# Kernel optimization log

Measured on AMD Instinct MI355X. Metric: run time of the kernel, lower is better.

The kernel has to match this reference:

```python
import jax, jax.numpy as jnp
import numpy as np

N = 50000   # node_count
D = 64      # dim_in (also GCN hidden, GRU hidden, top-k k)
E = 800000  # num_edges


def setup_inputs() -> dict:
    key = jax.random.key(0)
    ks = jax.random.split(key, 10)
    s = 1.0 / np.sqrt(D)
    return {
        "x": jax.random.normal(ks[0], (N, D), jnp.float32),
        "edge_index": jax.random.randint(ks[1], (2, E), 0, N, dtype=jnp.int64),
        "edge_weight": jax.random.uniform(ks[2], (E,), jnp.float32),
        # TopKPooling projection vector p
        "pool_p": jax.random.normal(ks[3], (D,), jnp.float32) * s,
        # EvolveGCNH initial weight (GRU hidden state h0), [D, D]
        "init_W": jax.random.normal(ks[4], (D, D), jnp.float32) * s,
        # GRU params, torch gate order (r, z, n)
        "gru_Wih": jax.random.normal(ks[5], (3 * D, D), jnp.float32) * s,
        "gru_Whh": jax.random.normal(ks[6], (3 * D, D), jnp.float32) * s,
        "gru_bih": jax.random.normal(ks[7], (3 * D,), jnp.float32) * s,
        "gru_bhh": jax.random.normal(ks[8], (3 * D,), jnp.float32) * s,
        # final Linear(D, 1)
        "lin_W": jax.random.normal(ks[9], (1, D), jnp.float32) * s,
        "lin_b": jnp.zeros((1,), jnp.float32),
    }


def reference(x, edge_index, edge_weight, pool_p, init_W,
              gru_Wih, gru_Whh, gru_bih, gru_bhh, lin_W, lin_b):
    n, d = x.shape
    # ---- TopKPooling: k = ceil((D/N) * N) = D nodes ----
    score = (x @ pool_p) / jnp.linalg.norm(pool_p)          # [N]
    vals, perm = jax.lax.top_k(score, d)                    # descending, k = D
    x_tilde = x[perm] * jnp.tanh(vals)[:, None]             # [D, D]
    # ---- one GRU step: batch = D pooled nodes, hidden = D, h0 = init_W ----
    gi = x_tilde @ gru_Wih.T + gru_bih                      # [D, 3D]
    gh = init_W @ gru_Whh.T + gru_bhh                       # [D, 3D]
    i_r, i_z, i_n = jnp.split(gi, 3, axis=-1)
    h_r, h_z, h_n = jnp.split(gh, 3, axis=-1)
    r = jax.nn.sigmoid(i_r + h_r)
    z = jax.nn.sigmoid(i_z + h_z)
    nn_ = jnp.tanh(i_n + r * h_n)
    W = (1.0 - z) * nn_ + z * init_W                        # evolved GCN weight [D, D]
    # ---- GCNConv_Fixed_W: add self-loops + symmetric norm + scatter ----
    loop = jnp.arange(n)
    row = jnp.concatenate([edge_index[0], loop])            # sources
    col = jnp.concatenate([edge_index[1], loop])            # targets
    w = jnp.concatenate([edge_weight, jnp.ones((n,), x.dtype)])
    deg = jax.ops.segment_sum(w, col, num_segments=n)
    deg_safe = jnp.where(deg > 0, deg, 1.0)
    dinv = jnp.where(deg > 0, jax.lax.rsqrt(deg_safe), 0.0)
    norm = dinv[row] * w * dinv[col]                        # [E+N]
    xw = x @ W                                              # [N, D]
    agg = jax.ops.segment_sum(norm[:, None] * xw[row], col, num_segments=n)
    # ---- head: relu + Linear(D, 1) ----
    h = jax.nn.relu(agg)
    return h @ lin_W.T + lin_b                              # [N, 1]
```

## Files before the change

kernel.cpp:

```cpp
#include <hip/hip_runtime.h>
#include <hip/hip_fp16.h>
#include <cmath>

#define N_NODES 50000
#define DIM 64
#define E_EDGES 800000
#define FIX32 65536.0f
#define NB_A 98
#define NB_EDGE 384
#define NRUNS 98
#define BUCKET 64
#define XW_BLOCKS 782

__device__ __forceinline__ void wave_sort64(float& v, int& idx, int lane) {
    #pragma unroll
    for (int k = 2; k <= 64; k <<= 1) {
        #pragma unroll
        for (int j = k >> 1; j > 0; j >>= 1) {
            float ov = __shfl_xor(v, j);
            int   oi = __shfl_xor(idx, j);
            bool lower = ((lane & j) == 0);
            bool up    = ((lane & k) == 0);
            bool mine_prec = (v > ov) || (v == ov && idx < oi);
            bool keep = up ? (lower == mine_prec) : (lower != mine_prec);
            if (!keep) { v = ov; idx = oi; }
        }
    }
}

__device__ __forceinline__ void wave_merge_top64(float& v, int& idx,
                                                 float bv, int bi, int lane) {
    bool a_prec = (v > bv) || (v == bv && idx < bi);
    if (!a_prec) { v = bv; idx = bi; }
    #pragma unroll
    for (int j = 32; j > 0; j >>= 1) {
        float ov = __shfl_xor(v, j);
        int   oi = __shfl_xor(idx, j);
        bool lower = ((lane & j) == 0);
        bool mine_prec = (v > ov) || (v == ov && idx < oi);
        bool keep = (lower == mine_prec);
        if (!keep) { v = ov; idx = oi; }
    }
}

__global__ __launch_bounds__(512) void score_topk_edge_kernel(
    const float* __restrict__ x, const float* __restrict__ p,
    float* __restrict__ cand_val, int* __restrict__ cand_idx,
    const int* __restrict__ ei, const float* __restrict__ ew,
    unsigned int* __restrict__ packed, unsigned int* __restrict__ ren) {
    __shared__ float sv[512];
    __shared__ int   si[512];
    int t = threadIdx.x, lane = t & 63, wvid = t >> 6;
    if (blockIdx.x < NB_A) {
        int g = blockIdx.x * 512 + t;
        float v; int idx;
        if (g < N_NODES) {
            const float4* x4 = (const float4*)(x + (size_t)g * DIM);
            const float4* p4 = (const float4*)p;
            float dot = 0.f, pn = 0.f;
            #pragma unroll
            for (int k = 0; k < 16; k++) {
                float4 xv = x4[k], pv = p4[k];
                dot += xv.x * pv.x + xv.y * pv.y + xv.z * pv.z + xv.w * pv.w;
                pn  += pv.x * pv.x + pv.y * pv.y + pv.z * pv.z + pv.w * pv.w;
            }
            v = dot / sqrtf(pn);
            idx = g;
        } else { v = -INFINITY; idx = 0x7fffffff; }
        wave_sort64(v, idx, lane);
        sv[t] = v; si[t] = idx;
        __syncthreads();
        if (wvid == 0) {
            #pragma unroll
            for (int r = 1; r < 8; r++)
                wave_merge_top64(v, idx, sv[r * 64 + 63 - lane], si[r * 64 + 63 - lane], lane);
            cand_val[blockIdx.x * 64 + lane] = v;
            cand_idx[blockIdx.x * 64 + lane] = idx;
        }
    }
    for (int e = blockIdx.x * 512 + t; e < E_EDGES; e += NB_EDGE * 512) {
        int r = ei[e], c = ei[E_EDGES + e];
        float wgt = ew[e];
        unsigned int q = (unsigned int)(wgt * FIX32);
        unsigned int old = atomicAdd(&packed[c], (1u << 24) | q);
        unsigned int pos = old >> 24;
        if (pos < BUCKET) {
            __half hw = __float2half(wgt);
            unsigned int rec = ((unsigned int)__half_as_ushort(hw) << 16) | (unsigned int)r;
            ren[(size_t)c * BUCKET + pos] = rec;
        }
    }
}

__global__ __launch_bounds__(1024) void topk_b_kernel(
    const float* __restrict__ cand_val, const int* __restrict__ cand_idx,
    const float* __restrict__ x, float* __restrict__ x_tilde) {
    __shared__ float rsv[16 * 64];
    __shared__ int   rsi[16 * 64];
    __shared__ float tval[64];
    __shared__ int   perm[64];
    int t = threadIdx.x, lane = t & 63, wv = t >> 6;
    int r0 = wv * 8;
    float v; int idx;
    if (r0 < NRUNS) { v = cand_val[r0 * 64 + lane]; idx = cand_idx[r0 * 64 + lane]; }
    else            { v = -INFINITY; idx = 0x7fffffff; }
    for (int r = r0 + 1; r < r0 + 8 && r < NRUNS; r++)
        wave_merge_top64(v, idx, cand_val[r * 64 + 63 - lane],
                         cand_idx[r * 64 + 63 - lane], lane);
    rsv[wv * 64 + lane] = v; rsi[wv * 64 + lane] = idx;
    __syncthreads();
    if (wv == 0) {
        v = rsv[lane]; idx = rsi[lane];
        for (int r = 1; r < 16; r++)
            wave_merge_top64(v, idx, rsv[r * 64 + 63 - lane],
                             rsi[r * 64 + 63 - lane], lane);
        tval[lane] = tanhf(v);
        perm[lane] = idx;
    }
    __syncthreads();
    for (int i = t; i < 4096; i += 1024) {
        int j = i >> 6, kk = i & 63;
        x_tilde[i] = x[perm[j] * DIM + kk] * tval[j];
    }
}

__global__ __launch_bounds__(256) void gru_kernel(
    const float* __restrict__ xt, const float* __restrict__ initW,
    const float* __restrict__ Wih, const float* __restrict__ Whh,
    const float* __restrict__ bih, const float* __restrict__ bhh,
    float* __restrict__ Wout) {
    __shared__ float xrow_s[256], hrow_s[256];
    int t = threadIdx.x;
    int i = blockIdx.x * 4 + (t >> 6);
    int j = t & 63;
    int li = (t >> 6) * 64 + j;
    xrow_s[li] = xt[i * 64 + j];
    hrow_s[li] = initW[i * 64 + j];
    __syncthreads();
    int lb = (t >> 6) * 64;
    float gi_r = bih[j], gi_z = bih[j + 64], gi_n = bih[j + 128];
    float gh_r = bhh[j], gh_z = bhh[j + 64], gh_n = bhh[j + 128];
    for (int k = 0; k < 64; k++) {
        float xv = xrow_s[lb + k], hv = hrow_s[lb + k];
        gi_r += xv * Wih[j * 64 + k];
        gi_z += xv * Wih[(j + 64) * 64 + k];
        gi_n += xv * Wih[(j + 128) * 64 + k];
        gh_r += hv * Whh[j * 64 + k];
        gh_z += hv * Whh[(j + 64) * 64 + k];
        gh_n += hv * Whh[(j + 128) * 64 + k];
    }
    float r = 1.f / (1.f + expf(-(gi_r + gh_r)));
    float z = 1.f / (1.f + expf(-(gi_z + gh_z)));
    float nn = tanhf(gi_n + r * gh_n);
    Wout[i * 64 + j] = (1.f - z) * nn + z * hrow_s[lb + j];
}

__global__ __launch_bounds__(256) void xw_kernel(
    const float* __restrict__ x, const float* __restrict__ W,
    const unsigned int* __restrict__ packed, __half* __restrict__ xwh) {
    __shared__ float Wl[64 * 64];
    __shared__ float Xl[64 * 64];
    __shared__ float dinv_s[64];
    int t = threadIdx.x;
    int r0 = blockIdx.x * 64;
    if (t < 64) {
        int r = r0 + t;
        unsigned int pk = (r < N_NODES) ? packed[r] : 0u;
        dinv_s[t] = rsqrtf((float)(pk & 0xFFFFFFu) * (1.0f / FIX32) + 1.0f);
    }
    for (int i = t; i < 4096; i += 256) Wl[i] = W[i];
    for (int i = t; i < 4096; i += 256) {
        int r = r0 + (i >> 6);
        Xl[i] = (r < N_NODES) ? x[r0 * 64 + i] : 0.f;
    }
    __syncthreads();
    int j = t & 63, ty = t >> 6;
    float acc[16];
    #pragma unroll
    for (int rr = 0; rr < 16; rr++) acc[rr] = 0.f;
    for (int k = 0; k < 64; k++) {
        float wvv = Wl[k * 64 + j];
        #pragma unroll
        for (int rr = 0; rr < 16; rr++)
            acc[rr] += Xl[(ty * 16 + rr) * 64 + k] * wvv;
    }
    #pragma unroll
    for (int rr = 0; rr < 16; rr++) {
        int r = r0 + ty * 16 + rr;
        if (r < N_NODES)
            xwh[r * DIM + j] = __float2half(acc[rr] * dinv_s[ty * 16 + rr]);
    }
}

__global__ __launch_bounds__(256) void gather_head_kernel(
    const unsigned int* __restrict__ packed, const unsigned int* __restrict__ ren,
    const float4* __restrict__ xwh,
    const float* __restrict__ linW, const float* __restrict__ linb,
    float* __restrict__ out) {
    int gid = blockIdx.x * blockDim.x + threadIdx.x;
    int n = gid >> 6, lane = gid & 63;
    if (n >= N_NODES) return;
    int c8 = lane & 7;
    int slot = lane >> 3;
    unsigned int pk = packed[n];
    int cnt = min((int)(pk >> 24), BUCKET);
    float di = rsqrtf((float)(pk & 0xFFFFFFu) * (1.0f / FIX32) + 1.0f);
    float acc[8];
    #pragma unroll
    for (int q = 0; q < 8; q++) acc[q] = 0.f;
    if (slot == 0) {
        float4 hv = xwh[n * 8 + c8];
        const __half2* h2 = reinterpret_cast<const __half2*>(&hv);
        #pragma unroll
        for (int q = 0; q < 4; q++) {
            float2 f = __half22float2(h2[q]);
            acc[2 * q]     = f.x;
            acc[2 * q + 1] = f.y;
        }
    }
    int rv = 0; float wv = 0.f;
    if (lane < cnt) {
        unsigned int rec = ren[(size_t)n * BUCKET + lane];
        rv = (int)(rec & 0xFFFFu);
        __half_raw hr; hr.x = (unsigned short)(rec >> 16);
        wv = __half2float(__half(hr));
    }
    int G = (cnt + 7) >> 3;
    int g = 0;
    for (; g + 2 <= G; g += 2) {
        int src0 = g * 8 + slot, src1 = src0 + 8;
        int   ra = __shfl(rv, src0);  float wa = __shfl(wv, src0);
        int   rb = __shfl(rv, src1);  float wb = __shfl(wv, src1);
        float4 ha = xwh[ra * 8 + c8];
        float4 hb = xwh[rb * 8 + c8];
        const __half2* h2a = reinterpret_cast<const __half2*>(&ha);
        const __half2* h2b = reinterpret_cast<const __half2*>(&hb);
        #pragma unroll
        for (int q = 0; q < 4; q++) {
            float2 fa = __half22float2(h2a[q]);
            float2 fb = __half22float2(h2b[q]);
            acc[2 * q]     += wa * fa.x + wb * fb.x;
            acc[2 * q + 1] += wa * fa.y + wb * fb.y;
        }
    }
    if (g < G) {
        int src = g * 8 + slot;
        int r = __shfl(rv, src);
        float ww = __shfl(wv, src);
        float4 hv = xwh[r * 8 + c8];
        const __half2* h2 = reinterpret_cast<const __half2*>(&hv);
        #pragma unroll
        for (int q = 0; q < 4; q++) {
            float2 f = __half22float2(h2[q]);
            acc[2 * q]     += ww * f.x;
            acc[2 * q + 1] += ww * f.y;
        }
    }
    #pragma unroll
    for (int q = 0; q < 8; q++) {
        acc[q] += __shfl_xor(acc[q], 8);
        acc[q] += __shfl_xor(acc[q], 16);
        acc[q] += __shfl_xor(acc[q], 32);
    }
    float pv = 0.f;
    #pragma unroll
    for (int q = 0; q < 8; q++)
        pv += fmaxf(di * acc[q], 0.f) * linW[c8 * 8 + q];
    pv += __shfl_xor(pv, 1); pv += __shfl_xor(pv, 2); pv += __shfl_xor(pv, 4);
    if (lane == 0) out[n] = pv + linb[0];
}

extern "C" void kernel_launch(void* const* d_in, const int* in_sizes, int n_in,
                              void* d_out, int out_size, void* d_ws, size_t ws_size,
                              hipStream_t stream) {
    const float* x     = (const float*)d_in[0];
    const int*   ei    = (const int*)d_in[1];
    const float* ew    = (const float*)d_in[2];
    const float* p     = (const float*)d_in[3];
    const float* initW = (const float*)d_in[4];
    const float* Wih   = (const float*)d_in[5];
    const float* Whh   = (const float*)d_in[6];
    const float* bih   = (const float*)d_in[7];
    const float* bhh   = (const float*)d_in[8];
    const float* linW  = (const float*)d_in[9];
    const float* linb  = (const float*)d_in[10];
    float* out = (float*)d_out;

    char* w = (char*)d_ws;
    unsigned int* packed = (unsigned int*)w; w += 4ull * N_NODES;
    unsigned int* ren = (unsigned int*)w;    w += 4ull * (size_t)N_NODES * BUCKET;
    __half* xwh    = (__half*)w;   w += 2ull * (size_t)N_NODES * DIM;
    float* cand_val= (float*)w;    w += 4ull * 8192;
    int*   cand_idx= (int*)w;      w += 4ull * 8192;
    float* x_tilde = (float*)w;    w += 4ull * 4096;
    float* W       = (float*)w;    w += 4ull * 4096;

    hipMemsetAsync(packed, 0, 4ull * N_NODES, stream);
    score_topk_edge_kernel<<<NB_EDGE, 512, 0, stream>>>(
        x, p, cand_val, cand_idx, ei, ew, packed, ren);
    topk_b_kernel<<<1, 1024, 0, stream>>>(cand_val, cand_idx, x, x_tilde);
    gru_kernel<<<16, 256, 0, stream>>>(x_tilde, initW, Wih, Whh, bih, bhh, W);
    xw_kernel<<<XW_BLOCKS, 256, 0, stream>>>(x, W, packed, xwh);
    gather_head_kernel<<<(N_NODES * 64 + 255) / 256, 256, 0, stream>>>(
        packed, ren, (const float4*)xwh, linW, linb, out);
}
```

Before: 205.5 us.

## Privatize edge bucketing per XCD with L2-scoped atomics

Each XCD gets its own copy of the per-node degree/count counters and edge buckets. Atomics are issued with an L2-scoped (sc0) inline asm instruction instead of device-scope atomics, which avoids cross-die coherence traffic. The xw and gather kernels now sum the eight partial degrees and build a prefix over the per-XCD counts to find each lane's edge record. In exchange, the counter memset is eight times larger, the gather does eight extra loads per node, and overflow handling changes: each XCD bucket is capped at 24 entries and the total at 64. The code also depends on the undocumented XCC_ID hardware register and waits on vmcnt after every atomic.

```diff
diff --git a/kernel.cpp b/kernel.cpp
--- a/kernel.cpp
+++ b/kernel.cpp
@@ -9,8 +9,23 @@
 #define NB_A 98
 #define NB_EDGE 384
 #define NRUNS 98
-#define BUCKET 64
+#define NXCD 8
+#define BUCKET8 24
 #define XW_BLOCKS 782
+
+__device__ __forceinline__ int xcc_id() {
+    int x;
+    asm volatile("s_getreg_b32 %0, hwreg(HW_REG_XCC_ID)" : "=s"(x));
+    return x & 7;
+}
+
+__device__ __forceinline__ unsigned int atomic_add_l2(unsigned int* addr, unsigned int val) {
+    unsigned int old;
+    asm volatile("global_atomic_add %0, %1, %2, off sc0\n\t"
+                 "s_waitcnt vmcnt(0)"
+                 : "=&v"(old) : "v"(addr), "v"(val) : "memory");
+    return old;
+}
 
 __device__ __forceinline__ void wave_sort64(float& v, int& idx, int lane) {
     #pragma unroll
@@ -47,7 +62,7 @@
     const float* __restrict__ x, const float* __restrict__ p,
     float* __restrict__ cand_val, int* __restrict__ cand_idx,
     const int* __restrict__ ei, const float* __restrict__ ew,
-    unsigned int* __restrict__ packed, unsigned int* __restrict__ ren) {
+    unsigned int* __restrict__ packed8, unsigned int* __restrict__ ren8) {
     __shared__ float sv[512];
     __shared__ int   si[512];
     int t = threadIdx.x, lane = t & 63, wvid = t >> 6;
@@ -78,16 +93,19 @@
             cand_idx[blockIdx.x * 64 + lane] = idx;
         }
     }
+    int xcc = xcc_id();
+    unsigned int* mypk = packed8 + (size_t)xcc * N_NODES;
+    unsigned int* myren = ren8 + (size_t)xcc * N_NODES * BUCKET8;
     for (int e = blockIdx.x * 512 + t; e < E_EDGES; e += NB_EDGE * 512) {
         int r = ei[e], c = ei[E_EDGES + e];
         float wgt = ew[e];
         unsigned int q = (unsigned int)(wgt * FIX32);
-        unsigned int old = atomicAdd(&packed[c], (1u << 24) | q);
+        unsigned int old = atomic_add_l2(&mypk[c], (1u << 24) | q);
         unsigned int pos = old >> 24;
-        if (pos < BUCKET) {
+        if (pos < BUCKET8) {
             __half hw = __float2half(wgt);
             unsigned int rec = ((unsigned int)__half_as_ushort(hw) << 16) | (unsigned int)r;
-            ren[(size_t)c * BUCKET + pos] = rec;
+            myren[(size_t)c * BUCKET8 + pos] = rec;
         }
     }
 }
@@ -157,7 +175,7 @@
 
 __global__ __launch_bounds__(256) void xw_kernel(
     const float* __restrict__ x, const float* __restrict__ W,
-    const unsigned int* __restrict__ packed, __half* __restrict__ xwh) {
+    const unsigned int* __restrict__ packed8, __half* __restrict__ xwh) {
     __shared__ float Wl[64 * 64];
     __shared__ float Xl[64 * 64];
     __shared__ float dinv_s[64];
@@ -165,8 +183,13 @@
     int r0 = blockIdx.x * 64;
     if (t < 64) {
         int r = r0 + t;
-        unsigned int pk = (r < N_NODES) ? packed[r] : 0u;
-        dinv_s[t] = rsqrtf((float)(pk & 0xFFFFFFu) * (1.0f / FIX32) + 1.0f);
+        unsigned int s = 0;
+        if (r < N_NODES) {
+            #pragma unroll
+            for (int xx = 0; xx < NXCD; xx++)
+                s += packed8[(size_t)xx * N_NODES + r] & 0xFFFFFFu;
+        }
+        dinv_s[t] = rsqrtf((float)s * (1.0f / FIX32) + 1.0f);
     }
     for (int i = t; i < 4096; i += 256) Wl[i] = W[i];
     for (int i = t; i < 4096; i += 256) {
@@ -193,7 +216,7 @@
 }
 
 __global__ __launch_bounds__(256) void gather_head_kernel(
-    const unsigned int* __restrict__ packed, const unsigned int* __restrict__ ren,
+    const unsigned int* __restrict__ packed8, const unsigned int* __restrict__ ren8,
     const float4* __restrict__ xwh,
     const float* __restrict__ linW, const float* __restrict__ linb,
     float* __restrict__ out) {
@@ -202,9 +225,18 @@
     if (n >= N_NODES) return;
     int c8 = lane & 7;
     int slot = lane >> 3;
-    unsigned int pk = packed[n];
-    int cnt = min((int)(pk >> 24), BUCKET);
-    float di = rsqrtf((float)(pk & 0xFFFFFFu) * (1.0f / FIX32) + 1.0f);
+    int xsel = -1, xslot = 0, pref = 0;
+    unsigned int wfix = 0;
+    #pragma unroll
+    for (int xx = 0; xx < NXCD; xx++) {
+        unsigned int pkx = packed8[(size_t)xx * N_NODES + n];
+        int cx = min((int)(pkx >> 24), BUCKET8);
+        wfix += pkx & 0xFFFFFFu;
+        if (lane >= pref && lane < pref + cx) { xsel = xx; xslot = lane - pref; }
+        pref += cx;
+    }
+    int cnt = min(pref, 64);
+    float di = rsqrtf((float)wfix * (1.0f / FIX32) + 1.0f);
     float acc[8];
     #pragma unroll
     for (int q = 0; q < 8; q++) acc[q] = 0.f;
@@ -219,8 +251,8 @@
         }
     }
     int rv = 0; float wv = 0.f;
-    if (lane < cnt) {
-        unsigned int rec = ren[(size_t)n * BUCKET + lane];
+    if (xsel >= 0 && lane < cnt) {
+        unsigned int rec = ren8[((size_t)xsel * N_NODES + n) * BUCKET8 + xslot];
         rv = (int)(rec & 0xFFFFu);
         __half_raw hr; hr.x = (unsigned short)(rec >> 16);
         wv = __half2float(__half(hr));
@@ -287,20 +319,20 @@
     float* out = (float*)d_out;
 
     char* w = (char*)d_ws;
-    unsigned int* packed = (unsigned int*)w; w += 4ull * N_NODES;
-    unsigned int* ren = (unsigned int*)w;    w += 4ull * (size_t)N_NODES * BUCKET;
+    unsigned int* packed8 = (unsigned int*)w; w += 4ull * NXCD * N_NODES;
+    unsigned int* ren8 = (unsigned int*)w;    w += 4ull * NXCD * N_NODES * BUCKET8;
     __half* xwh    = (__half*)w;   w += 2ull * (size_t)N_NODES * DIM;
     float* cand_val= (float*)w;    w += 4ull * 8192;
     int*   cand_idx= (int*)w;      w += 4ull * 8192;
     float* x_tilde = (float*)w;    w += 4ull * 4096;
     float* W       = (float*)w;    w += 4ull * 4096;
 
-    hipMemsetAsync(packed, 0, 4ull * N_NODES, stream);
+    hipMemsetAsync(packed8, 0, 4ull * NXCD * N_NODES, stream);
     score_topk_edge_kernel<<<NB_EDGE, 512, 0, stream>>>(
-        x, p, cand_val, cand_idx, ei, ew, packed, ren);
+        x, p, cand_val, cand_idx, ei, ew, packed8, ren8);
     topk_b_kernel<<<1, 1024, 0, stream>>>(cand_val, cand_idx, x, x_tilde);
     gru_kernel<<<16, 256, 0, stream>>>(x_tilde, initW, Wih, Whh, bih, bhh, W);
-    xw_kernel<<<XW_BLOCKS, 256, 0, stream>>>(x, W, packed, xwh);
+    xw_kernel<<<XW_BLOCKS, 256, 0, stream>>>(x, W, packed8, xwh);
     gather_head_kernel<<<(N_NODES * 64 + 255) / 256, 256, 0, stream>>>(
-        packed, ren, (const float4*)xwh, linW, linb, out);
-}
+        packed8, ren8, (const float4*)xwh, linW, linb, out);
+}
```

Result: no change. 208.7 us (+1.6%).
